# Performance work log

Hardware: AMD Instinct MI355X
Metric: run time of the kernel (lower is better)

Reference implementation:

```python
import jax, jax.numpy as jnp
import numpy as np

B, D, S, O = 32768, 1024, 64, 4  # batch, feature_dim, n_subjects, n_outputs


def setup_inputs() -> dict:
    key = jax.random.key(0)
    kx, ks, kw, kb = jax.random.split(key, 4)
    x = jax.random.normal(kx, (B, D), dtype=jnp.float32)          # backbone features
    subject_ids = jax.random.randint(ks, (B,), 0, S)              # per-sample head id
    W = jax.random.normal(kw, (S, D, O), dtype=jnp.float32) / np.float32(np.sqrt(D))
    b = jax.random.normal(kb, (S, O), dtype=jnp.float32) * 0.01
    return {"x": x, "subject_ids": subject_ids, "W": W, "b": b}


def reference(x, subject_ids, W, b):
    # Vectorized form of the per-subject loop:
    #   for sid in unique(subject_ids): outputs[idxs] = heads[sid](features[idxs])
    # Each head is Linear(D, O): out[i] = x[i] @ W[sid[i]] + b[sid[i]].
    Wg = jnp.take(W, subject_ids, axis=0)   # [B, D, O] gathered per-sample weights
    bg = jnp.take(b, subject_ids, axis=0)   # [B, O]
    return jnp.einsum('bd,bdo->bo', x, Wg) + bg
```

## Files before the change

### kernel.cpp

```cpp
#include <hip/hip_runtime.h>

constexpr int B = 32768;
constexpr int D = 1024;
constexpr int S = 64;
constexpr int O = 4;

constexpr int BLOCKS_PER_SID = 16;
constexpr int MAIN_BLOCKS    = S * BLOCKS_PER_SID;
constexpr int WAVES_PER_SID  = BLOCKS_PER_SID * 4;

constexpr int SORT_BLOCKS   = 64;
constexpr int ROWS_PER_SBLK = B / SORT_BLOCKS;

#define WS_OFFSETS 0
#define WS_BASE    128
#define WS_HIST    8192
#define WS_PERM    16384

__global__ __launch_bounds__(256) void hist_kernel(const int* __restrict__ sid,
                                                   int* __restrict__ ws) {
    __shared__ int h[S];
    const int t = threadIdx.x, b = blockIdx.x;
    if (t < S) h[t] = 0;
    __syncthreads();
    const int rbase = b * ROWS_PER_SBLK;
    atomicAdd(&h[sid[rbase + t]], 1);
    atomicAdd(&h[sid[rbase + 256 + t]], 1);
    __syncthreads();
    if (t < S) ws[WS_HIST + b * S + t] = h[t];
}

__global__ __launch_bounds__(64) void scan_kernel(int* __restrict__ ws) {
    __shared__ int tot[S];
    __shared__ int off[S + 1];
    const int s = threadIdx.x;
    int basev[SORT_BLOCKS];
    int acc = 0;
    #pragma unroll
    for (int b = 0; b < SORT_BLOCKS; ++b) {
        basev[b] = acc;
        acc += ws[WS_HIST + b * S + s];
    }
    tot[s] = acc;
    __syncthreads();
    if (s == 0) {
        int a = 0;
        for (int i = 0; i < S; ++i) { off[i] = a; a += tot[i]; }
        off[S] = a;
    }
    __syncthreads();
    const int o = off[s];
    ws[WS_OFFSETS + s] = o;
    if (s == 0) ws[WS_OFFSETS + S] = off[S];
    #pragma unroll
    for (int b = 0; b < SORT_BLOCKS; ++b)
        ws[WS_BASE + b * S + s] = basev[b] + o;
}

__global__ __launch_bounds__(256) void scatter_kernel(const int* __restrict__ sid,
                                                      int* __restrict__ ws) {
    __shared__ int cur[S];
    __shared__ int bas[S];
    const int t = threadIdx.x, b = blockIdx.x;
    if (t < S) { cur[t] = 0; bas[t] = ws[WS_BASE + b * S + t]; }
    __syncthreads();
    const int rbase = b * ROWS_PER_SBLK;
    const int i0 = rbase + t, i1 = rbase + 256 + t;
    const int s0 = sid[i0], s1 = sid[i1];
    const int r0 = atomicAdd(&cur[s0], 1);
    const int r1 = atomicAdd(&cur[s1], 1);
    ws[WS_PERM + bas[s0] + r0] = i0;
    ws[WS_PERM + bas[s1] + r1] = i1;
}

__global__ __launch_bounds__(256) void main_kernel(const float* __restrict__ x,
                                                   const float* __restrict__ W,
                                                   const float* __restrict__ bias,
                                                   const int* __restrict__ ws,
                                                   float* __restrict__ out) {
    __shared__ float4 Wl[D];

    const int s    = blockIdx.x / BLOCKS_PER_SID;
    const int blk  = blockIdx.x % BLOCKS_PER_SID;
    const int wave = threadIdx.x >> 6;
    const int lane = threadIdx.x & 63;

    const float4* __restrict__ Wg = (const float4*)(W + (size_t)s * (D * O));
    for (int d = threadIdx.x; d < D; d += 256) Wl[d] = Wg[d];
    __syncthreads();

    float4 w[4][4];
    #pragma unroll
    for (int k = 0; k < 4; ++k)
        #pragma unroll
        for (int j = 0; j < 4; ++j)
            w[k][j] = Wl[k * 256 + lane * 4 + j];

    const int start = ws[WS_OFFSETS + s];
    const int cnt   = ws[WS_OFFSETS + s + 1] - start;
    const int wv_id = blk * 4 + wave;

    const int   q  = (lane >> 2) & 3;
    const float bb = bias[s * O + q];

    int i   = wv_id;
    int row = (i < cnt) ? ws[WS_PERM + start + i] : 0;
    while (i < cnt) {
        const int i_next   = i + WAVES_PER_SID;
        const int row_next = (i_next < cnt) ? ws[WS_PERM + start + i_next] : 0;

        const float* __restrict__ xr = x + (size_t)row * D;
        float a0 = 0.f, a1 = 0.f, a2 = 0.f, a3 = 0.f;
        #pragma unroll
        for (int k = 0; k < 4; ++k) {
            const float4 xv = *(const float4*)(xr + k * 256 + lane * 4);
            a0 += xv.x * w[k][0].x + xv.y * w[k][1].x + xv.z * w[k][2].x + xv.w * w[k][3].x;
            a1 += xv.x * w[k][0].y + xv.y * w[k][1].y + xv.z * w[k][2].y + xv.w * w[k][3].y;
            a2 += xv.x * w[k][0].z + xv.y * w[k][1].z + xv.z * w[k][2].z + xv.w * w[k][3].z;
            a3 += xv.x * w[k][0].w + xv.y * w[k][1].w + xv.z * w[k][2].w + xv.w * w[k][3].w;
        }

        #pragma unroll
        for (int m = 4; m <= 32; m <<= 1) {
            a0 += __shfl_xor(a0, m, 64);
            a1 += __shfl_xor(a1, m, 64);
            a2 += __shfl_xor(a2, m, 64);
            a3 += __shfl_xor(a3, m, 64);
        }
        float v = (q == 0) ? a0 : (q == 1) ? a1 : (q == 2) ? a2 : a3;
        v += __shfl_xor(v, 1, 64);
        v += __shfl_xor(v, 2, 64);

        if (lane < 16 && (lane & 3) == 0)
            out[(size_t)row * O + q] = v + bb;

        i   = i_next;
        row = row_next;
    }
}

extern "C" void kernel_launch(void* const* d_in, const int* in_sizes, int n_in,
                              void* d_out, int out_size, void* d_ws, size_t ws_size,
                              hipStream_t stream) {
    const float* x    = (const float*)d_in[0];
    const int*   sid  = (const int*)d_in[1];
    const float* W    = (const float*)d_in[2];
    const float* bias = (const float*)d_in[3];
    float* out = (float*)d_out;
    int* ws = (int*)d_ws;

    hist_kernel   <<<SORT_BLOCKS, 256, 0, stream>>>(sid, ws);
    scan_kernel   <<<1,            64, 0, stream>>>(ws);
    scatter_kernel<<<SORT_BLOCKS, 256, 0, stream>>>(sid, ws);
    main_kernel   <<<MAIN_BLOCKS, 256, 0, stream>>>(x, W, bias, ws, out);
}
```

Before: 205.9 us.

## Software-pipeline x row loads, swizzle LDS weights, and cut shuffle reduction

The main kernel now loads the next row's x vectors before the cross-lane reduction of the current row, so global loads overlap the shuffles. Weights staged in LDS use an XOR swizzle to avoid bank conflicts when loaded into registers. The reduction is restructured: four shuffles are done on all four accumulators only at strides 16 and 32, then one selected value is reduced over strides 1-8. Launch bounds request occupancy 4, and the prefetch registers raise register pressure.

Result: no change. 204.4 us (-0.7%).

```diff
diff --git a/kernel.cpp b/kernel.cpp
--- a/kernel.cpp
+++ b/kernel.cpp
@@ -16,6 +16,8 @@
 #define WS_BASE    128
 #define WS_HIST    8192
 #define WS_PERM    16384
+
+__device__ __forceinline__ int swz(int e) { return e ^ ((e >> 3) & 7); }
 
 __global__ __launch_bounds__(256) void hist_kernel(const int* __restrict__ sid,
                                                    int* __restrict__ ws) {
@@ -73,11 +75,11 @@
     ws[WS_PERM + bas[s1] + r1] = i1;
 }
 
-__global__ __launch_bounds__(256) void main_kernel(const float* __restrict__ x,
-                                                   const float* __restrict__ W,
-                                                   const float* __restrict__ bias,
-                                                   const int* __restrict__ ws,
-                                                   float* __restrict__ out) {
+__global__ __launch_bounds__(256, 4) void main_kernel(const float* __restrict__ x,
+                                                      const float* __restrict__ W,
+                                                      const float* __restrict__ bias,
+                                                      const int* __restrict__ ws,
+                                                      float* __restrict__ out) {
     __shared__ float4 Wl[D];
 
     const int s    = blockIdx.x / BLOCKS_PER_SID;
@@ -86,7 +88,7 @@
     const int lane = threadIdx.x & 63;
 
     const float4* __restrict__ Wg = (const float4*)(W + (size_t)s * (D * O));
-    for (int d = threadIdx.x; d < D; d += 256) Wl[d] = Wg[d];
+    for (int e = threadIdx.x; e < D; e += 256) Wl[swz(e)] = Wg[e];
     __syncthreads();
 
     float4 w[4][4];
@@ -94,44 +96,72 @@
     for (int k = 0; k < 4; ++k)
         #pragma unroll
         for (int j = 0; j < 4; ++j)
-            w[k][j] = Wl[k * 256 + lane * 4 + j];
+            w[k][j] = Wl[swz(k * 256 + lane * 4 + j)];
 
     const int start = ws[WS_OFFSETS + s];
     const int cnt   = ws[WS_OFFSETS + s + 1] - start;
     const int wv_id = blk * 4 + wave;
 
-    const int   q  = (lane >> 2) & 3;
+    const int   q  = lane >> 4;
     const float bb = bias[s * O + q];
 
     int i   = wv_id;
     int row = (i < cnt) ? ws[WS_PERM + start + i] : 0;
+
+    float4 xv0, xv1, xv2, xv3;
+    if (i < cnt) {
+        const float* __restrict__ xr = x + (size_t)row * D;
+        xv0 = *(const float4*)(xr + 0 * 256 + lane * 4);
+        xv1 = *(const float4*)(xr + 1 * 256 + lane * 4);
+        xv2 = *(const float4*)(xr + 2 * 256 + lane * 4);
+        xv3 = *(const float4*)(xr + 3 * 256 + lane * 4);
+    }
+
     while (i < cnt) {
         const int i_next   = i + WAVES_PER_SID;
         const int row_next = (i_next < cnt) ? ws[WS_PERM + start + i_next] : 0;
 
-        const float* __restrict__ xr = x + (size_t)row * D;
-        float a0 = 0.f, a1 = 0.f, a2 = 0.f, a3 = 0.f;
-        #pragma unroll
-        for (int k = 0; k < 4; ++k) {
-            const float4 xv = *(const float4*)(xr + k * 256 + lane * 4);
-            a0 += xv.x * w[k][0].x + xv.y * w[k][1].x + xv.z * w[k][2].x + xv.w * w[k][3].x;
-            a1 += xv.x * w[k][0].y + xv.y * w[k][1].y + xv.z * w[k][2].y + xv.w * w[k][3].y;
-            a2 += xv.x * w[k][0].z + xv.y * w[k][1].z + xv.z * w[k][2].z + xv.w * w[k][3].z;
-            a3 += xv.x * w[k][0].w + xv.y * w[k][1].w + xv.z * w[k][2].w + xv.w * w[k][3].w;
+        float a0, a1, a2, a3;
+        {
+            a0  = xv0.x * w[0][0].x + xv0.y * w[0][1].x + xv0.z * w[0][2].x + xv0.w * w[0][3].x;
+            a1  = xv0.x * w[0][0].y + xv0.y * w[0][1].y + xv0.z * w[0][2].y + xv0.w * w[0][3].y;
+            a2  = xv0.x * w[0][0].z + xv0.y * w[0][1].z + xv0.z * w[0][2].z + xv0.w * w[0][3].z;
+            a3  = xv0.x * w[0][0].w + xv0.y * w[0][1].w + xv0.z * w[0][2].w + xv0.w * w[0][3].w;
+            a0 += xv1.x * w[1][0].x + xv1.y * w[1][1].x + xv1.z * w[1][2].x + xv1.w * w[1][3].x;
+            a1 += xv1.x * w[1][0].y + xv1.y * w[1][1].y + xv1.z * w[1][2].y + xv1.w * w[1][3].y;
+            a2 += xv1.x * w[1][0].z + xv1.y * w[1][1].z + xv1.z * w[1][2].z + xv1.w * w[1][3].z;
+            a3 += xv1.x * w[1][0].w + xv1.y * w[1][1].w + xv1.z * w[1][2].w + xv1.w * w[1][3].w;
+            a0 += xv2.x * w[2][0].x + xv2.y * w[2][1].x + xv2.z * w[2][2].x + xv2.w * w[2][3].x;
+            a1 += xv2.x * w[2][0].y + xv2.y * w[2][1].y + xv2.z * w[2][2].y + xv2.w * w[2][3].y;
+            a2 += xv2.x * w[2][0].z + xv2.y * w[2][1].z + xv2.z * w[2][2].z + xv2.w * w[2][3].z;
+            a3 += xv2.x * w[2][0].w + xv2.y * w[2][1].w + xv2.z * w[2][2].w + xv2.w * w[2][3].w;
+            a0 += xv3.x * w[3][0].x + xv3.y * w[3][1].x + xv3.z * w[3][2].x + xv3.w * w[3][3].x;
+            a1 += xv3.x * w[3][0].y + xv3.y * w[3][1].y + xv3.z * w[3][2].y + xv3.w * w[3][3].y;
+            a2 += xv3.x * w[3][0].z + xv3.y * w[3][1].z + xv3.z * w[3][2].z + xv3.w * w[3][3].z;
+            a3 += xv3.x * w[3][0].w + xv3.y * w[3][1].w + xv3.z * w[3][2].w + xv3.w * w[3][3].w;
+        }
+
+        if (i_next < cnt) {
+            const float* __restrict__ xn = x + (size_t)row_next * D;
+            xv0 = *(const float4*)(xn + 0 * 256 + lane * 4);
+            xv1 = *(const float4*)(xn + 1 * 256 + lane * 4);
+            xv2 = *(const float4*)(xn + 2 * 256 + lane * 4);
+            xv3 = *(const float4*)(xn + 3 * 256 + lane * 4);
         }
 
         #pragma unroll
-        for (int m = 4; m <= 32; m <<= 1) {
+        for (int m = 16; m <= 32; m <<= 1) {
             a0 += __shfl_xor(a0, m, 64);
             a1 += __shfl_xor(a1, m, 64);
             a2 += __shfl_xor(a2, m, 64);
             a3 += __shfl_xor(a3, m, 64);
         }
         float v = (q == 0) ? a0 : (q == 1) ? a1 : (q == 2) ? a2 : a3;
-        v += __shfl_xor(v, 1, 64);
-        v += __shfl_xor(v, 2, 64);
+        #pragma unroll
+        for (int m = 1; m <= 8; m <<= 1)
+            v += __shfl_xor(v, m, 64);
 
-        if (lane < 16 && (lane & 3) == 0)
+        if ((lane & 15) == 0)
             out[(size_t)row * O + q] = v + bb;
 
         i   = i_next;
```
